# Kernel optimization log

Measured on AMD Instinct MI355X. Metric: run time of the kernel, lower is better.

## Reference

```python
import jax, jax.numpy as jnp
import numpy as np

D, H, DH, FF = 768, 12, 64, 3072

def setup_inputs() -> dict:
    key = jax.random.key(0)
    ks = iter(jax.random.split(key, 40))
    B, Li, Lt = 128, 197, 64
    nrm = lambda shape, s=0.02: (jax.random.normal(next(ks), shape, jnp.float32) * s)
    inp = {}
    inp['image_feats'] = jax.random.normal(next(ks), (B, Li, D), jnp.float32)
    inp['image_att_score'] = jax.random.uniform(next(ks), (B, Li), jnp.float32)
    inp['text_feats'] = jax.random.normal(next(ks), (B, Lt, D), jnp.float32)
    inp['text_att_score'] = jax.random.uniform(next(ks), (B, Lt), jnp.float32)
    inp['tokens'] = jax.random.randint(next(ks), (B, Lt), 0, 1000)
    # BatchNorm1d bottlenecks (inference: running stats)
    for p in ('img', 'txt'):
        inp[f'bn_{p}_g'] = jnp.ones((D,), jnp.float32)
        inp[f'bn_{p}_b'] = jnp.zeros((D,), jnp.float32)
        inp[f'bn_{p}_m'] = nrm((D,), 0.1)
        inp[f'bn_{p}_v'] = jax.random.uniform(next(ks), (D,), jnp.float32, 0.5, 1.5)
    # ResidualAttention (1 layer, cross): ln1, ln2, qkv/out proj, mlp 768->3072->768
    inp['ln1_g'] = jnp.ones((D,), jnp.float32); inp['ln1_b'] = jnp.zeros((D,), jnp.float32)
    inp['ln2_g'] = jnp.ones((D,), jnp.float32); inp['ln2_b'] = jnp.zeros((D,), jnp.float32)
    for n in ('Wq', 'Wk', 'Wv', 'Wo'):
        inp[n] = nrm((D, D))
    for n in ('bq', 'bk', 'bv', 'bo'):
        inp[n] = jnp.zeros((D,), jnp.float32)
    inp['W1'] = nrm((D, FF)); inp['b1'] = jnp.zeros((FF,), jnp.float32)
    inp['W2'] = nrm((FF, D)); inp['b2'] = jnp.zeros((D,), jnp.float32)
    inp['img_K'] = 59   # int(197 * 0.3)
    inp['text_K'] = 19  # int(64 * 0.3)
    return inp

def _ln(x, g, b):
    mu = jnp.mean(x, -1, keepdims=True)
    v = jnp.mean((x - mu) ** 2, -1, keepdims=True)
    return (x - mu) * jax.lax.rsqrt(v + 1e-5) * g + b

def _bn(x, g, b, m, v):
    return (x - m) * jax.lax.rsqrt(v + 1e-5) * g + b

def _cross_block(x, y, key_mask, ln1_g, ln1_b, ln2_g, ln2_b,
                 Wq, bq, Wk, bk, Wv, bv, Wo, bo, W1, b1, W2, b2):
    # cross-attn: queries from x, keys/values from y; pre-LN residual block
    B, Lq, _ = x.shape
    Lk = y.shape[1]
    qn = _ln(x, ln1_g, ln1_b)
    kn = _ln(y, ln1_g, ln1_b)
    q = (qn @ Wq + bq).reshape(B, Lq, H, DH)
    k = (kn @ Wk + bk).reshape(B, Lk, H, DH)
    v = (kn @ Wv + bv).reshape(B, Lk, H, DH)
    scores = jnp.einsum('bqhd,bkhd->bhqk', q, k) / np.float32(np.sqrt(DH))
    if key_mask is not None:  # True = padding -> masked out
        scores = jnp.where(key_mask[:, None, None, :], jnp.float32(-1e9), scores)
    a = jax.nn.softmax(scores, axis=-1)
    att = jnp.einsum('bhqk,bkhd->bqhd', a, v).reshape(B, Lq, D) @ Wo + bo
    x = x + att
    h = _ln(x, ln2_g, ln2_b)
    x = x + jax.nn.gelu(h @ W1 + b1, approximate=False) @ W2 + b2
    return x

def _select(feats, score, K):
    # zero CLS score, full descending sort via top_k, gather token subsets
    L = score.shape[1]
    score = score * jnp.concatenate([jnp.zeros_like(score[:, :1]), jnp.ones_like(score[:, 1:])], axis=1)
    _, idx = jax.lax.top_k(score, L)  # [B, L] sorted desc
    cls = feats[:, :1, :]
    sel1 = jnp.take_along_axis(feats, idx[:, :K, None], axis=1)
    sel2 = jnp.take_along_axis(feats, idx[:, K:2 * K, None], axis=1)
    return jnp.concatenate([cls, sel1], 1), jnp.concatenate([cls, sel2], 1)

def reference(image_feats, image_att_score, text_feats, text_att_score, tokens,
              bn_img_g, bn_img_b, bn_img_m, bn_img_v,
              bn_txt_g, bn_txt_b, bn_txt_m, bn_txt_v,
              ln1_g, ln1_b, ln2_g, ln2_b,
              Wq, bq, Wk, bk, Wv, bv, Wo, bo, W1, b1, W2, b2,
              img_K, text_K):
    blk = lambda x, y, m: _cross_block(x, y, m, ln1_g, ln1_b, ln2_g, ln2_b,
                                       Wq, bq, Wk, bk, Wv, bv, Wo, bo, W1, b1, W2, b2)
    img_global = _bn(image_feats[:, 0, :], bn_img_g, bn_img_b, bn_img_m, bn_img_v)
    text_global = _bn(text_feats[:, 0, :], bn_txt_g, bn_txt_b, bn_txt_m, bn_txt_v)
    text_masks = (tokens == 0)  # True where padding
    img_sel1, img_sel2 = _select(image_feats, image_att_score, img_K)
    image_part1 = blk(img_sel1, image_feats, None)
    image_part2 = blk(img_sel2, image_feats, None)
    txt_sel1, txt_sel2 = _select(text_feats, text_att_score, text_K)
    text_part1 = blk(txt_sel1, text_feats, text_masks)
    text_part2 = blk(txt_sel2, text_feats, text_masks)
    return (img_global, text_global, image_part1, image_part2, text_part1, text_part2)
```

## Files before the change

kernel.cpp:

```cpp
#include <hip/hip_runtime.h>

typedef unsigned short u16;
typedef __bf16 bf16x8 __attribute__((ext_vector_type(8)));
typedef float f32x4 __attribute__((ext_vector_type(4)));

__device__ __forceinline__ float b2f(u16 u) { return __builtin_bit_cast(float, (unsigned)u << 16); }
__device__ __forceinline__ u16 f2b(float f) {
  unsigned x = __builtin_bit_cast(unsigned, f);
  x += 0x7fffu + ((x >> 16) & 1u);
  return (u16)(x >> 16);
}

__device__ __forceinline__ void gload16(const u16* g, u16* l) {
  auto gp = (__attribute__((address_space(1))) void*)(void*)const_cast<u16*>(g);
  auto lp = (__attribute__((address_space(3))) void*)(void*)l;
  __builtin_amdgcn_global_load_lds(gp, lp, 16, 0, 0);
}

__device__ __forceinline__ f32x4 mfma16(bf16x8 a, bf16x8 b, f32x4 c) {
  return __builtin_amdgcn_mfma_f32_16x16x32_bf16(a, b, c, 0, 0, 0);
}

__device__ __forceinline__ float gelu_fast(float v) {
  float u = v * (0.7978845608028654f + 0.03567740813636141f * v * v);
  float e = __expf(2.0f * u);
  float th = 1.0f - 2.0f / (e + 1.0f);
  return 0.5f * v * (1.0f + th);
}

__global__ __launch_bounds__(256) void transpose_k(const float* __restrict__ in, u16* __restrict__ out,
                                                   int R, int C) {
  __shared__ float tile[32][33];
  const int bx = blockIdx.x * 32, by = blockIdx.y * 32;
  const int x = threadIdx.x;
  for (int yy = threadIdx.y; yy < 32; yy += 8) tile[yy][x] = in[(size_t)(by + yy) * C + bx + x];
  __syncthreads();
  for (int yy = threadIdx.y; yy < 32; yy += 8) out[(size_t)(bx + yy) * R + by + x] = f2b(tile[x][yy]);
}

__global__ __launch_bounds__(256) void bn_kernel(const float* __restrict__ feats, int Lrow,
                                                 const float* g, const float* b, const float* m, const float* v,
                                                 float* __restrict__ out) {
  const int bb = blockIdx.x;
  const float* row = feats + (size_t)bb * Lrow * 768;
  for (int d = threadIdx.x; d < 768; d += 256) {
    float x = row[d];
    out[bb * 768 + d] = (x - m[d]) * (1.0f / sqrtf(v[d] + 1e-5f)) * g[d] + b[d];
  }
}

__global__ __launch_bounds__(256) void topk_sel(const float* __restrict__ score, int L, int Ksel,
                                                int* __restrict__ sel, int Lq) {
  __shared__ float s[256];
  const int b = blockIdx.x;
  const int stride2 = 128 * Lq;
  for (int i = threadIdx.x; i < L; i += 256) {
    float v = score[b * L + i];
    s[i] = (i == 0) ? 0.0f : v;
  }
  __syncthreads();
  for (int i = threadIdx.x; i < L; i += 256) {
    float si = s[i];
    int rank = 0;
    for (int j = 0; j < L; ++j) {
      float sj = s[j];
      rank += (sj > si) || (sj == si && j < i);
    }
    if (rank < Ksel) sel[b * Lq + rank + 1] = i;
    else if (rank < 2 * Ksel) sel[stride2 + b * Lq + (rank - Ksel) + 1] = i;
  }
  if (threadIdx.x == 0) { sel[b * Lq] = 0; sel[stride2 + b * Lq] = 0; }
}

__global__ __launch_bounds__(256) void ln_rows(const float* __restrict__ x, const float* g, const float* b,
                                               u16* __restrict__ out) {
  const int row = blockIdx.x * 4 + (threadIdx.x >> 6);
  const int l = threadIdx.x & 63;
  const float* xr = x + (size_t)row * 768;
  float v[12]; float s = 0.f;
#pragma unroll
  for (int i = 0; i < 12; ++i) { v[i] = xr[l + i * 64]; s += v[i]; }
  for (int d = 1; d < 64; d <<= 1) s += __shfl_xor(s, d);
  const float mu = s * (1.0f / 768.0f);
  float q = 0.f;
#pragma unroll
  for (int i = 0; i < 12; ++i) { float t = v[i] - mu; q += t * t; }
  for (int d = 1; d < 64; d <<= 1) q += __shfl_xor(q, d);
  const float rs = 1.0f / sqrtf(q * (1.0f / 768.0f) + 1e-5f);
#pragma unroll
  for (int i = 0; i < 12; ++i) {
    int c = l + i * 64;
    out[(size_t)row * 768 + c] = f2b((v[i] - mu) * rs * g[c] + b[c]);
  }
}

__global__ __launch_bounds__(128) void gather_kernel(const int* __restrict__ sel, const u16* __restrict__ kn,
                                                     const float* __restrict__ feats, u16* __restrict__ qn,
                                                     float* __restrict__ xs, int Lq, int Lsrc) {
  const int q = blockIdx.x, by = blockIdx.y;
  const int p = by >> 7, b = by & 127;
  const int row = (p * 128 + b) * Lq + q;
  const int src = sel[row];
  const uint4* sq = (const uint4*)(kn + ((size_t)b * Lsrc + src) * 768);
  uint4* dq = (uint4*)(qn + (size_t)row * 768);
  for (int c = threadIdx.x; c < 96; c += 128) dq[c] = sq[c];
  const float4* sx = (const float4*)(feats + ((size_t)b * Lsrc + src) * 768);
  float4* dx = (float4*)(xs + (size_t)row * 768);
  for (int c = threadIdx.x; c < 192; c += 128) dx[c] = sx[c];
}

enum { EPI_PLAIN = 0, EPI_QSCALE = 1, EPI_GELU = 2, EPI_RES_FADD = 3, EPI_RES_OUT = 4 };

__device__ __forceinline__ void epi_store(int EPI_ignored, float v, size_t off, void* outp, const float* res);

template <int EPI>
__device__ __forceinline__ void epi_write(float v, size_t off, void* outp, const float* res) {
  if constexpr (EPI == EPI_QSCALE) {
    ((u16*)outp)[off] = f2b(v * 0.125f);
  } else if constexpr (EPI == EPI_GELU) {
    ((u16*)outp)[off] = f2b(gelu_fast(v));
  } else if constexpr (EPI == EPI_RES_FADD || EPI == EPI_RES_OUT) {
    ((float*)outp)[off] = v + res[off];
  } else {
    ((u16*)outp)[off] = f2b(v);
  }
}

template <int EPI>
__global__ __launch_bounds__(256) void gemm_bt(const u16* __restrict__ A, const u16* __restrict__ Bt,
                                               const float* __restrict__ bias, const float* __restrict__ res,
                                               void* __restrict__ outp, int M, int N, int K) {
  __shared__ alignas(16) u16 As[2][128 * 64];
  __shared__ alignas(16) u16 Bs[2][128 * 64];
  const int tid = threadIdx.x, l = tid & 63, w = tid >> 6;
  const int nwg = gridDim.x * gridDim.y;
  int lin = blockIdx.y * gridDim.x + blockIdx.x;
  const int q8 = nwg >> 3, r8 = nwg & 7;
  const int xcd = lin & 7, pos = lin >> 3;
  const int nl = (xcd < r8) ? (xcd * (q8 + 1) + pos) : (r8 * (q8 + 1) + (xcd - r8) * q8 + pos);
  const int m0 = (nl / gridDim.x) * 128, n0 = (nl % gridDim.x) * 128;
  const int wm = (w & 1) * 64, wn = (w >> 1) * 64;
  f32x4 acc[4][4] = {};

  auto STAGE = [&](int buf, int k0) {
#pragma unroll
    for (int p = 0; p < 4; ++p) {
      const int s = p * 256 + tid;
      const int row = s >> 3, ch = (s & 7) ^ (row & 7);
      gload16(A + (size_t)(m0 + row) * K + k0 + ch * 8, &As[buf][s * 8]);
      gload16(Bt + (size_t)(n0 + row) * K + k0 + ch * 8, &Bs[buf][s * 8]);
    }
  };
  auto COMPUTE = [&](int buf) {
#pragma unroll
    for (int kk = 0; kk < 2; ++kk) {
      bf16x8 af[4], bfr[4];
#pragma unroll
      for (int i = 0; i < 4; ++i) {
        const int arow = wm + i * 16 + (l & 15);
        af[i] = *(const bf16x8*)&As[buf][arow * 64 + ((((kk * 4 + (l >> 4))) ^ (arow & 7)) << 3)];
        const int brow = wn + i * 16 + (l & 15);
        bfr[i] = *(const bf16x8*)&Bs[buf][brow * 64 + ((((kk * 4 + (l >> 4))) ^ (brow & 7)) << 3)];
      }
      __builtin_amdgcn_s_setprio(1);
#pragma unroll
      for (int mi = 0; mi < 4; ++mi)
#pragma unroll
        for (int ni = 0; ni < 4; ++ni) acc[mi][ni] = mfma16(af[mi], bfr[ni], acc[mi][ni]);
      __builtin_amdgcn_s_setprio(0);
    }
  };

  const int NT = K >> 6;
  STAGE(0, 0);
  int cur = 0;
  for (int t = 0; t < NT - 1; ++t) {
    STAGE(cur ^ 1, (t + 1) << 6);
    asm volatile("s_waitcnt vmcnt(8)" ::: "memory");
    __builtin_amdgcn_sched_barrier(0);
    __builtin_amdgcn_s_barrier();
    COMPUTE(cur);
    __builtin_amdgcn_s_barrier();
    cur ^= 1;
  }
  asm volatile("s_waitcnt vmcnt(0)" ::: "memory");
  __builtin_amdgcn_sched_barrier(0);
  __builtin_amdgcn_s_barrier();
  COMPUTE(cur);

  const int r4 = (l >> 4) * 4, c16 = l & 15;
#pragma unroll
  for (int mi = 0; mi < 4; ++mi)
#pragma unroll
    for (int ni = 0; ni < 4; ++ni) {
      const int gn = n0 + wn + ni * 16 + c16;
      const float bia = bias[gn];
#pragma unroll
      for (int j = 0; j < 4; ++j) {
        const int gm = m0 + wm + mi * 16 + r4 + j;
        epi_write<EPI>(acc[mi][ni][j] + bia, (size_t)gm * N + gn, outp, res);
      }
    }
}

template <int EPI>
__global__ __launch_bounds__(512, 2) void gemm256(const u16* __restrict__ A, const u16* __restrict__ Bt,
                                                  const float* __restrict__ bias, const float* __restrict__ res,
                                                  void* __restrict__ outp, int M, int N, int K) {
  __shared__ alignas(16) u16 As[2][256 * 64];
  __shared__ alignas(16) u16 Bs[2][256 * 64];
  const int tid = threadIdx.x, l = tid & 63, w = tid >> 6;
  const int nwg = gridDim.x * gridDim.y;
  int lin = blockIdx.y * gridDim.x + blockIdx.x;
  const int q8 = nwg >> 3, r8 = nwg & 7;
  const int xcd = lin & 7, pos = lin >> 3;
  const int nl = (xcd < r8) ? (xcd * (q8 + 1) + pos) : (r8 * (q8 + 1) + (xcd - r8) * q8 + pos);
  const int m0 = (nl / gridDim.x) * 256, n0 = (nl % gridDim.x) * 256;
  const int wr = w >> 2, wc = w & 3;
  f32x4 acc[8][4] = {};

  auto STAGE = [&](int buf, int k0) {
#pragma unroll
    for (int i = 0; i < 4; ++i) {
      const int s = i * 512 + tid;
      const int row = s >> 3, ch = (s & 7) ^ (row & 7);
      gload16(A + (size_t)(m0 + row) * K + k0 + ch * 8, &As[buf][s * 8]);
    }
#pragma unroll
    for (int i = 0; i < 4; ++i) {
      const int s = i * 512 + tid;
      const int row = s >> 3, ch = (s & 7) ^ (row & 7);
      gload16(Bt + (size_t)(n0 + row) * K + k0 + ch * 8, &Bs[buf][s * 8]);
    }
  };

  auto COMPUTE = [&](int buf) {
#pragma unroll
    for (int kk = 0; kk < 2; ++kk) {
      bf16x8 bfr[4], af[8];
#pragma unroll
      for (int j = 0; j < 4; ++j) {
        const int brow = wc * 64 + j * 16 + (l & 15);
        bfr[j] = *(const bf16x8*)&Bs[buf][brow * 64 + (((kk * 4 + (l >> 4)) ^ (brow & 7)) << 3)];
      }
#pragma unroll
      for (int i = 0; i < 8; ++i) {
        const int arow = wr * 128 + i * 16 + (l & 15);
        af[i] = *(const bf16x8*)&As[buf][arow * 64 + (((kk * 4 + (l >> 4)) ^ (arow & 7)) << 3)];
      }
      __builtin_amdgcn_s_setprio(1);
#pragma unroll
      for (int i = 0; i < 8; ++i)
#pragma unroll
        for (int j = 0; j < 4; ++j) acc[i][j] = mfma16(af[i], bfr[j], acc[i][j]);
      __builtin_amdgcn_s_setprio(0);
    }
  };

  const int NT = K >> 6;
  STAGE(0, 0);
  STAGE(1, 64);
  for (int t = 0; t < NT; ++t) {
    if (t < NT - 1) {
      asm volatile("s_waitcnt vmcnt(8)" ::: "memory");
    } else {
      asm volatile("s_waitcnt vmcnt(0)" ::: "memory");
    }
    __builtin_amdgcn_sched_barrier(0);
    __builtin_amdgcn_s_barrier();
    COMPUTE(t & 1);
    __builtin_amdgcn_s_barrier();
    if (t + 2 < NT) STAGE(t & 1, (t + 2) << 6);
  }

  const int r4 = (l >> 4) * 4, c16 = l & 15;
#pragma unroll
  for (int i = 0; i < 8; ++i)
#pragma unroll
    for (int j = 0; j < 4; ++j) {
      const int gn = n0 + wc * 64 + j * 16 + c16;
      const float bia = bias[gn];
#pragma unroll
      for (int jj = 0; jj < 4; ++jj) {
        const int gm = m0 + wr * 128 + i * 16 + r4 + jj;
        epi_write<EPI>(acc[i][j][jj] + bia, (size_t)gm * N + gn, outp, res);
      }
    }
}

template <int LQP, int LKP, int LQ, int LK, bool MASK>
__global__ __launch_bounds__(256) void attn2(const u16* __restrict__ Q, const u16* __restrict__ Kb,
                                             const u16* __restrict__ Vb, const int* __restrict__ toks,
                                             u16* __restrict__ O) {
  constexpr int LKS = LKP + 8;
  const int h = blockIdx.x, by = blockIdx.y;
  const int p = by & 1, bb = by >> 1;
  const int tid = threadIdx.x, l = tid & 63, w = tid >> 6;
  const size_t qrow0 = (size_t)(p * 128 + bb) * LQ;
  const u16* Qg = Q + qrow0 * 768 + h * 64;
  const u16* Kg = Kb + (size_t)bb * LK * 768 + h * 64;
  const u16* Vg = Vb + (size_t)bb * LK * 768 + h * 64;

  __shared__ alignas(16) u16 Qs[LQP * 64];
  __shared__ alignas(16) u16 KV[64 * LKS];
  __shared__ alignas(16) u16 Ss[LQP * LKS];
  __shared__ int tokLds[MASK ? LKP : 1];

  for (int s = tid; s < LQP * 8; s += 256) {
    int row = s >> 3, d8 = (s & 7) ^ (row & 7);
    int gr = row < LQ ? row : LQ - 1;
    gload16(Qg + (size_t)gr * 768 + d8 * 8, &Qs[s * 8]);
  }
  for (int s = tid; s < LKP * 8; s += 256) {
    int row = s >> 3, d8 = (s & 7) ^ (row & 7);
    int gr = row < LK ? row : LK - 1;
    gload16(Kg + (size_t)gr * 768 + d8 * 8, &KV[s * 8]);
  }
  if (MASK)
    for (int c = tid; c < LKP; c += 256) tokLds[c] = (c < LK) ? toks[bb * LK + c] : 1;
  __syncthreads();

  for (int nt = w; nt < LKP / 16; nt += 4) {
    const int brow = nt * 16 + (l & 15);
#pragma unroll
    for (int mt = 0; mt < LQP / 16; ++mt) {
      const int arow = mt * 16 + (l & 15);
      f32x4 a_ = {0.f, 0.f, 0.f, 0.f};
#pragma unroll
      for (int kk = 0; kk < 2; ++kk) {
        bf16x8 av = *(const bf16x8*)&Qs[arow * 64 + (((kk * 4 + (l >> 4)) ^ (arow & 7)) << 3)];
        bf16x8 bv = *(const bf16x8*)&KV[brow * 64 + (((kk * 4 + (l >> 4)) ^ (brow & 7)) << 3)];
        a_ = mfma16(av, bv, a_);
      }
      const int r0 = mt * 16 + (l >> 4) * 4, cc = nt * 16 + (l & 15);
#pragma unroll
      for (int j = 0; j < 4; ++j) Ss[(r0 + j) * LKS + cc] = f2b(a_[j]);
    }
  }
  __syncthreads();

  {
    const int kcol = tid & 31, d8 = tid >> 5;
#pragma unroll
    for (int kb = 0; kb < LKP / 32; ++kb) {
      const int k = kb * 32 + kcol;
      alignas(16) u16 tmp[8] = {0, 0, 0, 0, 0, 0, 0, 0};
      if (k < LK) *(uint4*)tmp = *(const uint4*)(Vg + (size_t)k * 768 + d8 * 8);
#pragma unroll
      for (int j = 0; j < 8; ++j) KV[(d8 * 8 + j) * LKS + k] = tmp[j];
    }
  }
  constexpr int NCH = (LKP + 63) / 64;
  for (int r = w; r < LQ; r += 4) {
    float sv[NCH];
    float mx = -INFINITY;
#pragma unroll
    for (int i = 0; i < NCH; ++i) {
      int c = l + (i << 6);
      float s = -INFINITY;
      if (c < LK) {
        s = b2f(Ss[r * LKS + c]);
        if (MASK && tokLds[c] == 0) s = -1e9f;
      }
      sv[i] = s;
      mx = fmaxf(mx, s);
    }
    for (int d = 1; d < 64; d <<= 1) mx = fmaxf(mx, __shfl_xor(mx, d));
    float sum = 0.f;
#pragma unroll
    for (int i = 0; i < NCH; ++i) { float e = __expf(sv[i] - mx); sv[i] = e; sum += e; }
    for (int d = 1; d < 64; d <<= 1) sum += __shfl_xor(sum, d);
    const float inv = 1.0f / sum;
#pragma unroll
    for (int i = 0; i < NCH; ++i) {
      int c = l + (i << 6);
      if (c < LKP) Ss[r * LKS + c] = f2b(sv[i] * inv);
    }
  }
  __syncthreads();

  for (int mt = w; mt < LQP / 16; mt += 4) {
    const int arow = mt * 16 + (l & 15);
#pragma unroll
    for (int nt = 0; nt < 4; ++nt) {
      f32x4 a_ = {0.f, 0.f, 0.f, 0.f};
#pragma unroll
      for (int kk = 0; kk < LKP; kk += 32) {
        bf16x8 av = *(const bf16x8*)&Ss[arow * LKS + kk + (l >> 4) * 8];
        bf16x8 bv = *(const bf16x8*)&KV[(nt * 16 + (l & 15)) * LKS + kk + (l >> 4) * 8];
        a_ = mfma16(av, bv, a_);
      }
      const int r0 = mt * 16 + (l >> 4) * 4, c16 = l & 15;
#pragma unroll
      for (int j = 0; j < 4; ++j) {
        int r = r0 + j;
        if (r < LQ) O[(qrow0 + r) * 768 + h * 64 + nt * 16 + c16] = f2b(a_[j]);
      }
    }
  }
}

extern "C" void kernel_launch(void* const* d_in, const int* in_sizes, int n_in,
                              void* d_out, int out_size, void* d_ws, size_t ws_size,
                              hipStream_t stream) {
  (void)in_sizes; (void)n_in; (void)out_size; (void)ws_size;
  const float* image_feats = (const float*)d_in[0];
  const float* image_att = (const float*)d_in[1];
  const float* text_feats = (const float*)d_in[2];
  const float* text_att = (const float*)d_in[3];
  const int* tokens = (const int*)d_in[4];
  const float* bn_img_g = (const float*)d_in[5];
  const float* bn_img_b = (const float*)d_in[6];
  const float* bn_img_m = (const float*)d_in[7];
  const float* bn_img_v = (const float*)d_in[8];
  const float* bn_txt_g = (const float*)d_in[9];
  const float* bn_txt_b = (const float*)d_in[10];
  const float* bn_txt_m = (const float*)d_in[11];
  const float* bn_txt_v = (const float*)d_in[12];
  const float* ln1_g = (const float*)d_in[13];
  const float* ln1_b = (const float*)d_in[14];
  const float* ln2_g = (const float*)d_in[15];
  const float* ln2_b = (const float*)d_in[16];
  const float* Wq = (const float*)d_in[17];
  const float* Wk = (const float*)d_in[18];
  const float* Wv = (const float*)d_in[19];
  const float* Wo = (const float*)d_in[20];
  const float* bq = (const float*)d_in[21];
  const float* bk = (const float*)d_in[22];
  const float* bv = (const float*)d_in[23];
  const float* bo = (const float*)d_in[24];
  const float* W1 = (const float*)d_in[25];
  const float* b1 = (const float*)d_in[26];
  const float* W2 = (const float*)d_in[27];
  const float* b2 = (const float*)d_in[28];

  float* out = (float*)d_out;
  char* wsp = (char*)d_ws;
  size_t off = 0;
  auto alloc = [&](size_t bytes) -> void* {
    void* p = wsp + off;
    off += (bytes + 255) & ~(size_t)255;
    return p;
  };
  u16* WqT = (u16*)alloc(768 * 768 * 2);
  u16* WkT = (u16*)alloc(768 * 768 * 2);
  u16* WvT = (u16*)alloc(768 * 768 * 2);
  u16* WoT = (u16*)alloc(768 * 768 * 2);
  u16* W1T = (u16*)alloc((size_t)768 * 3072 * 2);
  u16* W2T = (u16*)alloc((size_t)768 * 3072 * 2);
  char* kvbase = (char*)(wsp + off);
  u16* kn_i = (u16*)alloc((size_t)25344 * 768 * 2);
  u16* Kb_i = (u16*)alloc((size_t)25344 * 768 * 2);
  u16* Vb_i = (u16*)alloc((size_t)25344 * 768 * 2);
  u16* kn_t = (u16*)alloc((size_t)8192 * 768 * 2);
  u16* Kb_t = (u16*)alloc((size_t)8192 * 768 * 2);
  u16* Vb_t = (u16*)alloc((size_t)8192 * 768 * 2);
  u16* gb = (u16*)kvbase;
  int* sel_i = (int*)alloc(2 * 128 * 60 * 4);
  int* sel_t = (int*)alloc(2 * 128 * 20 * 4);
  u16* qn = (u16*)alloc((size_t)20480 * 768 * 2);
  float* xs = (float*)alloc((size_t)20480 * 768 * 4);
  u16* Qb = (u16*)alloc((size_t)20480 * 768 * 2);

  const dim3 tb(32, 8);
  transpose_k<<<dim3(24, 24), tb, 0, stream>>>(Wq, WqT, 768, 768);
  transpose_k<<<dim3(24, 24), tb, 0, stream>>>(Wk, WkT, 768, 768);
  transpose_k<<<dim3(24, 24), tb, 0, stream>>>(Wv, WvT, 768, 768);
  transpose_k<<<dim3(24, 24), tb, 0, stream>>>(Wo, WoT, 768, 768);
  transpose_k<<<dim3(96, 24), tb, 0, stream>>>(W1, W1T, 768, 3072);
  transpose_k<<<dim3(24, 96), tb, 0, stream>>>(W2, W2T, 3072, 768);

  bn_kernel<<<128, 256, 0, stream>>>(image_feats, 197, bn_img_g, bn_img_b, bn_img_m, bn_img_v, out);
  bn_kernel<<<128, 256, 0, stream>>>(text_feats, 64, bn_txt_g, bn_txt_b, bn_txt_m, bn_txt_v, out + 98304);

  topk_sel<<<128, 256, 0, stream>>>(image_att, 197, 59, sel_i, 60);
  topk_sel<<<128, 256, 0, stream>>>(text_att, 64, 19, sel_t, 20);

  ln_rows<<<25216 / 4, 256, 0, stream>>>(image_feats, ln1_g, ln1_b, kn_i);
  gemm256<EPI_PLAIN><<<dim3(3, 99), 512, 0, stream>>>(kn_i, WkT, bk, nullptr, Kb_i, 25344, 768, 768);
  gemm256<EPI_PLAIN><<<dim3(3, 99), 512, 0, stream>>>(kn_i, WvT, bv, nullptr, Vb_i, 25344, 768, 768);
  ln_rows<<<8192 / 4, 256, 0, stream>>>(text_feats, ln1_g, ln1_b, kn_t);
  gemm_bt<EPI_PLAIN><<<dim3(6, 64), 256, 0, stream>>>(kn_t, WkT, bk, nullptr, Kb_t, 8192, 768, 768);
  gemm_bt<EPI_PLAIN><<<dim3(6, 64), 256, 0, stream>>>(kn_t, WvT, bv, nullptr, Vb_t, 8192, 768, 768);

  gather_kernel<<<dim3(60, 256), 128, 0, stream>>>(sel_i, kn_i, image_feats, qn, xs, 60, 197);
  gather_kernel<<<dim3(20, 256), 128, 0, stream>>>(sel_t, kn_t, text_feats, qn + (size_t)15360 * 768,
                                                   xs + (size_t)15360 * 768, 20, 64);

  gemm256<EPI_QSCALE><<<dim3(3, 80), 512, 0, stream>>>(qn, WqT, bq, nullptr, Qb, 20480, 768, 768);

  attn2<64, 224, 60, 197, false><<<dim3(12, 256), 256, 0, stream>>>(Qb, Kb_i, Vb_i, nullptr, qn);
  attn2<32, 64, 20, 64, true><<<dim3(12, 256), 256, 0, stream>>>(Qb + (size_t)15360 * 768, Kb_t, Vb_t,
                                                                 tokens, qn + (size_t)15360 * 768);

  gemm256<EPI_RES_FADD><<<dim3(3, 80), 512, 0, stream>>>(qn, WoT, bo, xs, xs, 20480, 768, 768);
  ln_rows<<<20480 / 4, 256, 0, stream>>>(xs, ln2_g, ln2_b, Qb);
  gemm256<EPI_GELU><<<dim3(12, 80), 512, 0, stream>>>(Qb, W1T, b1, nullptr, gb, 20480, 3072, 768);
  gemm256<EPI_RES_OUT><<<dim3(3, 80), 512, 0, stream>>>(gb, W2T, b2, xs, out + 196608, 20480, 768, 3072);
}
```

Baseline: 813.5 us.

## Restructure gemm256 into 4-stage K=32 pipeline with single barrier per step

The 256x256 GEMM now uses four LDS buffers of 32-wide K slices instead of two 64-wide ones, keeping three tiles in flight. Each step has one barrier instead of two. Global-to-LDS loads for tile t+3 are issued between the two halves of the MFMA work, so copies overlap with compute. The LDS layout and swizzle are remapped so that each 64-element LDS row packs two 128-row halves. The aim is to hide memory latency and cut barrier stalls, at the cost of finer-grained wait counting and a more intricate address mapping.

```diff
diff --git a/kernel.cpp b/kernel.cpp
--- a/kernel.cpp
+++ b/kernel.cpp
@@ -110,8 +110,6 @@
 }
 
 enum { EPI_PLAIN = 0, EPI_QSCALE = 1, EPI_GELU = 2, EPI_RES_FADD = 3, EPI_RES_OUT = 4 };
-
-__device__ __forceinline__ void epi_store(int EPI_ignored, float v, size_t off, void* outp, const float* res);
 
 template <int EPI>
 __device__ __forceinline__ void epi_write(float v, size_t off, void* outp, const float* res) {
@@ -207,8 +205,8 @@
 __global__ __launch_bounds__(512, 2) void gemm256(const u16* __restrict__ A, const u16* __restrict__ Bt,
                                                   const float* __restrict__ bias, const float* __restrict__ res,
                                                   void* __restrict__ outp, int M, int N, int K) {
-  __shared__ alignas(16) u16 As[2][256 * 64];
-  __shared__ alignas(16) u16 Bs[2][256 * 64];
+  __shared__ alignas(16) u16 As[4][128 * 64];
+  __shared__ alignas(16) u16 Bs[4][128 * 64];
   const int tid = threadIdx.x, l = tid & 63, w = tid >> 6;
   const int nwg = gridDim.x * gridDim.y;
   int lin = blockIdx.y * gridDim.x + blockIdx.x;
@@ -217,60 +215,69 @@
   const int nl = (xcd < r8) ? (xcd * (q8 + 1) + pos) : (r8 * (q8 + 1) + (xcd - r8) * q8 + pos);
   const int m0 = (nl / gridDim.x) * 256, n0 = (nl % gridDim.x) * 256;
   const int wr = w >> 2, wc = w & 3;
+  const u16* Ab = A + (size_t)m0 * K;
+  const u16* Bb = Bt + (size_t)n0 * K;
   f32x4 acc[8][4] = {};
 
-  auto STAGE = [&](int buf, int k0) {
-#pragma unroll
-    for (int i = 0; i < 4; ++i) {
-      const int s = i * 512 + tid;
-      const int row = s >> 3, ch = (s & 7) ^ (row & 7);
-      gload16(A + (size_t)(m0 + row) * K + k0 + ch * 8, &As[buf][s * 8]);
-    }
-#pragma unroll
-    for (int i = 0; i < 4; ++i) {
-      const int s = i * 512 + tid;
-      const int row = s >> 3, ch = (s & 7) ^ (row & 7);
-      gload16(Bt + (size_t)(n0 + row) * K + k0 + ch * 8, &Bs[buf][s * 8]);
-    }
+  auto STG = [&](const u16* base, u16* lds, int k0, int p) {
+    const int s = p * 512 + tid;
+    const int lrow = s >> 3;
+    const int v = (s & 7) ^ (lrow & 7);
+    gload16(base + (size_t)(lrow + (v >> 2) * 128) * K + k0 + (v & 3) * 8, lds + s * 8);
   };
-
-  auto COMPUTE = [&](int buf) {
-#pragma unroll
-    for (int kk = 0; kk < 2; ++kk) {
-      bf16x8 bfr[4], af[8];
-#pragma unroll
-      for (int j = 0; j < 4; ++j) {
-        const int brow = wc * 64 + j * 16 + (l & 15);
-        bfr[j] = *(const bf16x8*)&Bs[buf][brow * 64 + (((kk * 4 + (l >> 4)) ^ (brow & 7)) << 3)];
-      }
-#pragma unroll
-      for (int i = 0; i < 8; ++i) {
-        const int arow = wr * 128 + i * 16 + (l & 15);
-        af[i] = *(const bf16x8*)&As[buf][arow * 64 + (((kk * 4 + (l >> 4)) ^ (arow & 7)) << 3)];
-      }
+  const int aoff = (l & 15) * 64 + ((((l >> 4) | (wr << 2)) ^ (l & 7)) << 3);
+  const int boff = ((wc & 1) * 64 + (l & 15)) * 64 + ((((l >> 4) | ((wc >> 1) << 2)) ^ (l & 7)) << 3);
+
+  const int NT = K >> 5;
+#pragma unroll
+  for (int pt = 0; pt < 3; ++pt) {
+    STG(Ab, As[pt], pt << 5, 0);
+    STG(Ab, As[pt], pt << 5, 1);
+    STG(Bb, Bs[pt], pt << 5, 0);
+    STG(Bb, Bs[pt], pt << 5, 1);
+  }
+
+  for (int t = 0; t < NT; ++t) {
+    const int buf = t & 3;
+    if (t <= NT - 3) {
+      asm volatile("s_waitcnt vmcnt(8)" ::: "memory");
+    } else if (t == NT - 2) {
+      asm volatile("s_waitcnt vmcnt(4)" ::: "memory");
+    } else {
+      asm volatile("s_waitcnt vmcnt(0)" ::: "memory");
+    }
+    __builtin_amdgcn_sched_barrier(0);
+    __builtin_amdgcn_s_barrier();
+    __builtin_amdgcn_sched_barrier(0);
+    const bool stg = (t + 3 < NT);
+    const int sbuf = (t + 3) & 3, sk = (t + 3) << 5;
+    bf16x8 bfr[4];
+    if (stg) { STG(Ab, As[sbuf], sk, 0); STG(Bb, Bs[sbuf], sk, 0); }
+#pragma unroll
+    for (int j = 0; j < 4; ++j) bfr[j] = *(const bf16x8*)&Bs[buf][boff + j * 1024];
+    {
+      bf16x8 af[4];
+#pragma unroll
+      for (int i = 0; i < 4; ++i) af[i] = *(const bf16x8*)&As[buf][aoff + i * 1024];
       __builtin_amdgcn_s_setprio(1);
 #pragma unroll
-      for (int i = 0; i < 8; ++i)
+      for (int i = 0; i < 4; ++i)
 #pragma unroll
         for (int j = 0; j < 4; ++j) acc[i][j] = mfma16(af[i], bfr[j], acc[i][j]);
       __builtin_amdgcn_s_setprio(0);
     }
-  };
-
-  const int NT = K >> 6;
-  STAGE(0, 0);
-  STAGE(1, 64);
-  for (int t = 0; t < NT; ++t) {
-    if (t < NT - 1) {
-      asm volatile("s_waitcnt vmcnt(8)" ::: "memory");
-    } else {
-      asm volatile("s_waitcnt vmcnt(0)" ::: "memory");
-    }
-    __builtin_amdgcn_sched_barrier(0);
-    __builtin_amdgcn_s_barrier();
-    COMPUTE(t & 1);
-    __builtin_amdgcn_s_barrier();
-    if (t + 2 < NT) STAGE(t & 1, (t + 2) << 6);
+    if (stg) { STG(Ab, As[sbuf], sk, 1); STG(Bb, Bs[sbuf], sk, 1); }
+    {
+      bf16x8 af[4];
+#pragma unroll
+      for (int i = 0; i < 4; ++i) af[i] = *(const bf16x8*)&As[buf][aoff + (i + 4) * 1024];
+      __builtin_amdgcn_s_setprio(1);
+#pragma unroll
+      for (int i = 0; i < 4; ++i)
+#pragma unroll
+        for (int j = 0; j < 4; ++j) acc[i + 4][j] = mfma16(af[i], bfr[j], acc[i + 4][j]);
+      __builtin_amdgcn_s_setprio(0);
+    }
   }
 
   const int r4 = (l >> 4) * 4, c16 = l & 15;
```

Result: slower. 889.1 us (+9.3%).
